# Kernel optimization log

Measured on AMD Instinct MI355X. Metric: run time of the kernel, lower is better.

## Reference

```python
import jax, jax.numpy as jnp
import numpy as np

LR_POS = 0.45   # adj_lr_pos: max(i/iters - 1, 0.45) == 0.45 always
LR_SIZE = 0.4
ITERS = 5
BOARD = 640.0


def box_iou(a, b):
    """Pairwise IoU. a: [..., N, 4], b: [..., M, 4] in pascal_voc -> [..., N, M]."""
    area_a = (a[..., 2] - a[..., 0]) * (a[..., 3] - a[..., 1])
    area_b = (b[..., 2] - b[..., 0]) * (b[..., 3] - b[..., 1])
    lt = jnp.maximum(a[..., :, None, :2], b[..., None, :, :2])
    rb = jnp.minimum(a[..., :, None, 2:], b[..., None, :, 2:])
    wh = jnp.clip(rb - lt, 0.0)
    inter = wh[..., 0] * wh[..., 1]
    union = area_a[..., :, None] + area_b[..., None, :] - inter
    return inter / union


def _make_boxes(key, shape, scale):
    # valid pascal_voc boxes: x1<x2, y1<y2
    corners = jax.random.uniform(key, shape[:-1] + (2, 2), dtype=jnp.float32)
    lo = jnp.min(corners, axis=-2)
    hi = jnp.max(corners, axis=-2) + 0.01  # avoid degenerate zero-area boxes
    return jnp.concatenate([lo, hi], axis=-1) * scale


def setup_inputs() -> dict:
    key = jax.random.key(0)
    k1, k2 = jax.random.split(key)
    B, N, M = 64, 1000, 100
    boxes = _make_boxes(k1, (B, N, 4), BOARD)
    gt_boxes = _make_boxes(k2, (B, M, 4), BOARD)
    return {"boxes": boxes, "gt_boxes": gt_boxes}


def reference(boxes, gt_boxes):
    """Batched progressive box adjustment toward best-IoU ground truth.

    boxes: [B, N, 4], gt_boxes: [B, M, 4], both pascal_voc.
    Returns (all_boxes [B, ITERS+1, N, 4], all_sims [B, ITERS+1, N, M]).
    """
    iou0 = box_iou(boxes, gt_boxes)  # [B, N, M]

    def step(carry, _):
        b, iou = carry
        best = jnp.argmax(iou, axis=-1)                                   # [B, N]
        best_gt = jnp.take_along_axis(gt_boxes, best[..., None], axis=1)  # [B, N, 4]
        cur_center = (b[..., :2] + b[..., 2:]) / 2
        gt_center = (best_gt[..., :2] + best_gt[..., 2:]) / 2
        delta_center = gt_center - cur_center
        delta_size = (best_gt[..., 2:] - best_gt[..., :2]) - (b[..., 2:] - b[..., :2])
        new_lt = b[..., :2] + LR_POS * delta_center
        new_rb = b[..., 2:] + LR_POS * delta_center + LR_SIZE * (delta_size - delta_center)
        new_b = jnp.concatenate([new_lt, new_rb], axis=-1)
        new_iou = box_iou(new_b, gt_boxes)
        return (new_b, new_iou), (new_b, new_iou)

    _, (boxes_seq, iou_seq) = jax.lax.scan(step, (boxes, iou0), None, length=ITERS)
    # prepend initial state: [ITERS+1, B, ...] -> [B, ITERS+1, ...]
    all_boxes = jnp.concatenate([boxes[None], boxes_seq], axis=0).transpose(1, 0, 2, 3)
    all_sims = jnp.concatenate([iou0[None], iou_seq], axis=0).transpose(1, 0, 2, 3)
    return all_boxes, all_sims
```

## Files before the change

### kernel.cpp

```cpp
#include <hip/hip_runtime.h>


#define BB 64
#define NN 1000
#define MM 100
#define NITER 5

__global__ __launch_bounds__(128, 8) void dvg_kernel(
    const float* __restrict__ boxes, const float* __restrict__ gt,
    float* __restrict__ out) {
  __shared__ float4 lgt[MM];

  const int tid = threadIdx.x;
  const int wv = tid >> 6;
  const int lane = tid & 63;
  const int r = lane >> 2;
  const int g = lane & 3;
  const int b = blockIdx.x >> 5;
  const int n0 = (blockIdx.x & 31) * 32 + wv * 16;
  const int n = n0 + r;
  const bool vrow = n < NN;
  const int nc = vrow ? n : NN - 1;

  for (int i = tid; i < MM; i += 128)
    lgt[i] = reinterpret_cast<const float4*>(gt)[b * MM + i];
  __syncthreads();

  const float4 bx = reinterpret_cast<const float4*>(boxes)[b * NN + nc];
  float b0 = bx.x, b1 = bx.y, b2 = bx.z, b3 = bx.w;

  float* __restrict__ outB = out;
  float* __restrict__ outS = out + (size_t)BB * 6 * NN * 4;

  for (int it = 0;; ++it) {
    asm volatile("" ::: "memory");

    float area = (b2 - b0) * (b3 - b1);
    asm("" : "+v"(area));

    float best = -1.0f;
    int bim = 0;
    const size_t obase = (size_t)(b * 6 + it) * NN + n0;
    float* __restrict__ os = outS + obase * MM + (size_t)r * MM;

#pragma unroll
    for (int k = 0; k < 7; ++k) {
      if (k < 6 || g == 0) {
        float4 d;
#pragma unroll
        for (int c = 0; c < 4; ++c) {
          const int m = 16 * k + 4 * g + c;
          const float4 q = lgt[m];
          float ag = (q.z - q.x) * (q.w - q.y);
          asm("" : "+v"(ag));
          const float w = fmaxf(fminf(b2, q.z) - fmaxf(b0, q.x), 0.0f);
          const float h = fmaxf(fminf(b3, q.w) - fmaxf(b1, q.y), 0.0f);
          float inter = w * h;
          asm("" : "+v"(inter));
          const float uni = (area + ag) - inter;
          const float val = inter * __builtin_amdgcn_rcpf(uni);
          (&d.x)[c] = val;
          const bool t = val > best;
          best = t ? val : best;
          bim = t ? m : bim;
        }
        if (vrow) *reinterpret_cast<float4*>(os + 16 * k + 4 * g) = d;
      }
    }

    if (vrow) {
      const float comp = g == 0 ? b0 : (g == 1 ? b1 : (g == 2 ? b2 : b3));
      outB[obase * 4 + lane] = comp;
    }
    if (it == NITER) break;

#pragma unroll
    for (int off = 1; off <= 2; off <<= 1) {
      const float ov = __shfl_xor(best, off, 64);
      const int obi = __shfl_xor(bim, off, 64);
      const bool t = (ov > best) || (ov == best && obi < bim);
      best = t ? ov : best;
      bim = t ? obi : bim;
    }

    const float4 gg = lgt[bim];
    const float dcx = (gg.x + gg.z) * 0.5f - (b0 + b2) * 0.5f;
    const float dcy = (gg.y + gg.w) * 0.5f - (b1 + b3) * 0.5f;
    const float dsx = (gg.z - gg.x) - (b2 - b0);
    const float dsy = (gg.w - gg.y) - (b3 - b1);
    float px = 0.45f * dcx;
    asm("" : "+v"(px));
    float py = 0.45f * dcy;
    asm("" : "+v"(py));
    float qx = 0.4f * (dsx - dcx);
    asm("" : "+v"(qx));
    float qy = 0.4f * (dsy - dcy);
    asm("" : "+v"(qy));
    b0 = b0 + px;
    b1 = b1 + py;
    b2 = (b2 + px) + qx;
    b3 = (b3 + py) + qy;
  }
}

extern "C" void kernel_launch(void* const* d_in, const int* in_sizes, int n_in,
                              void* d_out, int out_size, void* d_ws,
                              size_t ws_size, hipStream_t stream) {
  const float* boxes = (const float*)d_in[0];
  const float* gt = (const float*)d_in[1];
  float* out = (float*)d_out;
  dvg_kernel<<<BB * 32, 128, 0, stream>>>(boxes, gt, out);
}
```

Baseline: 38.60 us.

## Split each box row across two lanes instead of four, halving grid size

Result: slower. 56.26 us (+45.7%).

```diff
diff --git a/kernel.cpp b/kernel.cpp
--- a/kernel.cpp
+++ b/kernel.cpp
@@ -6,24 +6,22 @@
 #define MM 100
 #define NITER 5
 
-__global__ __launch_bounds__(128, 8) void dvg_kernel(
+__global__ __launch_bounds__(128) void dvg_kernel(
     const float* __restrict__ boxes, const float* __restrict__ gt,
     float* __restrict__ out) {
   __shared__ float4 lgt[MM];
 
   const int tid = threadIdx.x;
-  const int wv = tid >> 6;
   const int lane = tid & 63;
-  const int r = lane >> 2;
-  const int g = lane & 3;
-  const int b = blockIdx.x >> 5;
-  const int n0 = (blockIdx.x & 31) * 32 + wv * 16;
-  const int n = n0 + r;
+  const int p = lane & 1;
+  const int i = tid >> 1;
+  const int b = blockIdx.x >> 4;
+  const int n = (blockIdx.x & 15) * 64 + i;
   const bool vrow = n < NN;
   const int nc = vrow ? n : NN - 1;
 
-  for (int i = tid; i < MM; i += 128)
-    lgt[i] = reinterpret_cast<const float4*>(gt)[b * MM + i];
+  for (int t = tid; t < MM; t += 128)
+    lgt[t] = reinterpret_cast<const float4*>(gt)[b * MM + t];
   __syncthreads();
 
   const float4 bx = reinterpret_cast<const float4*>(boxes)[b * NN + nc];
@@ -32,25 +30,24 @@
   float* __restrict__ outB = out;
   float* __restrict__ outS = out + (size_t)BB * 6 * NN * 4;
 
+  const int mbase = p ? 52 : 0;
+
   for (int it = 0;; ++it) {
-    asm volatile("" ::: "memory");
-
     float area = (b2 - b0) * (b3 - b1);
     asm("" : "+v"(area));
 
     float best = -1.0f;
     int bim = 0;
-    const size_t obase = (size_t)(b * 6 + it) * NN + n0;
-    float* __restrict__ os = outS + obase * MM + (size_t)r * MM;
+    float* __restrict__ osr = outS + ((size_t)(b * 6 + it) * NN + n) * MM + mbase;
 
 #pragma unroll
-    for (int k = 0; k < 7; ++k) {
-      if (k < 6 || g == 0) {
+    for (int c = 0; c < 13; ++c) {
+      if (p == 0 || c < 12) {
+        const int ms = mbase + 4 * c;
         float4 d;
 #pragma unroll
-        for (int c = 0; c < 4; ++c) {
-          const int m = 16 * k + 4 * g + c;
-          const float4 q = lgt[m];
+        for (int u = 0; u < 4; ++u) {
+          const float4 q = lgt[ms + u];
           float ag = (q.z - q.x) * (q.w - q.y);
           asm("" : "+v"(ag));
           const float w = fmaxf(fminf(b2, q.z) - fmaxf(b0, q.x), 0.0f);
@@ -59,25 +56,24 @@
           asm("" : "+v"(inter));
           const float uni = (area + ag) - inter;
           const float val = inter * __builtin_amdgcn_rcpf(uni);
-          (&d.x)[c] = val;
+          (&d.x)[u] = val;
           const bool t = val > best;
           best = t ? val : best;
-          bim = t ? m : bim;
+          bim = t ? ms + u : bim;
         }
-        if (vrow) *reinterpret_cast<float4*>(os + 16 * k + 4 * g) = d;
+        if (vrow) *reinterpret_cast<float4*>(osr + 4 * c) = d;
       }
     }
 
-    if (vrow) {
-      const float comp = g == 0 ? b0 : (g == 1 ? b1 : (g == 2 ? b2 : b3));
-      outB[obase * 4 + lane] = comp;
+    if (vrow && p == 0) {
+      reinterpret_cast<float4*>(outB)[(size_t)(b * 6 + it) * NN + n] =
+          make_float4(b0, b1, b2, b3);
     }
     if (it == NITER) break;
 
-#pragma unroll
-    for (int off = 1; off <= 2; off <<= 1) {
-      const float ov = __shfl_xor(best, off, 64);
-      const int obi = __shfl_xor(bim, off, 64);
+    {
+      const float ov = __shfl_xor(best, 1, 64);
+      const int obi = __shfl_xor(bim, 1, 64);
       const bool t = (ov > best) || (ov == best && obi < bim);
       best = t ? ov : best;
       bim = t ? obi : bim;
@@ -109,5 +105,5 @@
   const float* boxes = (const float*)d_in[0];
   const float* gt = (const float*)d_in[1];
   float* out = (float*)d_out;
-  dvg_kernel<<<BB * 32, 128, 0, stream>>>(boxes, gt, out);
+  dvg_kernel<<<BB * 16, 128, 0, stream>>>(boxes, gt, out);
 }
```
